# Kernel optimization log

Hardware: AMD Instinct MI355X
Metric: run time of the kernel (lower is better)

Reference implementation:

```python
import jax, jax.numpy as jnp
import numpy as np

TREE_DEPTH = 10
TOTAL = 2 ** (TREE_DEPTH + 1) - 1  # 2047 nodes per tree
G = 64                              # graphs per batch
N = G * TOTAL                       # 131008 nodes
E = 2 * N                           # 262016 directed edges
H = 256                             # h_dim
HALF = H // 2
L = 4                               # num_layers
LABELS = 32
OUT = 32
BN_EPS = 1e-5
LN_EPS = 1e-5


def setup_inputs() -> dict:
    key = jax.random.key(0)
    ks = jax.random.split(key, 16)
    x = jnp.stack([jax.random.randint(ks[0], (N,), 0, TOTAL),
                   jax.random.randint(ks[1], (N,), 0, LABELS)], axis=1)
    edge_src = jax.random.randint(ks[2], (E,), 0, N)
    edge_dst = jax.random.randint(ks[3], (E,), 0, N)
    edge_weight = jax.random.uniform(ks[4], (E,), dtype=jnp.float32)
    batch = jnp.arange(N, dtype=jnp.int64) // TOTAL          # node -> graph id
    root_index = jnp.arange(G, dtype=jnp.int64) * TOTAL      # one root per graph
    s = 0.02
    emb_node = jax.random.normal(ks[5], (TOTAL, HALF), dtype=jnp.float32) * s
    emb_label = jax.random.normal(ks[6], (LABELS, HALF), dtype=jnp.float32) * s
    w = 1.0 / np.sqrt(H)
    W1 = jax.random.normal(ks[7], (L, H, H), dtype=jnp.float32) * w
    b1 = jnp.zeros((L, H), dtype=jnp.float32)
    g1 = jnp.ones((L, H), dtype=jnp.float32)
    be1 = jnp.zeros((L, H), dtype=jnp.float32)
    W2 = jax.random.normal(ks[8], (L, H, H), dtype=jnp.float32) * w
    b2 = jnp.zeros((L, H), dtype=jnp.float32)
    g2 = jnp.ones((L, H), dtype=jnp.float32)
    be2 = jnp.zeros((L, H), dtype=jnp.float32)
    ln_g = jnp.ones((L, H), dtype=jnp.float32)
    ln_b = jnp.zeros((L, H), dtype=jnp.float32)
    Wout = jax.random.normal(ks[9], (OUT, H), dtype=jnp.float32) * w
    return {"x": x, "edge_src": edge_src, "edge_dst": edge_dst,
            "edge_weight": edge_weight, "batch": batch, "root_index": root_index,
            "emb_node": emb_node, "emb_label": emb_label,
            "W1": W1, "b1": b1, "g1": g1, "be1": be1,
            "W2": W2, "b2": b2, "g2": g2, "be2": be2,
            "ln_g": ln_g, "ln_b": ln_b, "Wout": Wout}


def _batchnorm(h, g, b):
    # BatchNorm1d, training-mode batch statistics over the node dim
    m = h.mean(axis=0)
    v = h.var(axis=0)
    return g * (h - m) * jax.lax.rsqrt(v + BN_EPS) + b


def _layernorm(h, g, b):
    m = h.mean(axis=-1, keepdims=True)
    v = h.var(axis=-1, keepdims=True)
    return g * (h - m) * jax.lax.rsqrt(v + LN_EPS) + b


def reference(x, edge_src, edge_dst, edge_weight, batch, root_index,
              emb_node, emb_label, W1, b1, g1, be1, W2, b2, g2, be2,
              ln_g, ln_b, Wout):
    # BiEmbedding_cat: concat of two h/2 embeddings
    h = jnp.concatenate([emb_node[x[:, 0]], emb_label[x[:, 1]]], axis=-1)  # [N,H]
    target_roots = root_index[batch]  # all-nodes->root targets for last layer
    for i in range(L):
        if i == L - 1:  # last_layer_fully_adjacent: every node sends to its root
            agg = jnp.zeros_like(h).at[target_roots].add(h)
        else:
            agg = jnp.zeros_like(h).at[edge_dst].add(h[edge_src] * edge_weight[:, None])
        m = h + agg  # GIN with eps=0: (1+eps)*x + sum_j w_ij x_j
        m = jax.nn.relu(_batchnorm(m @ W1[i].T + b1[i], g1[i], be1[i]))
        m = jax.nn.relu(_batchnorm(m @ W2[i].T + b2[i], g2[i], be2[i]))
        # use_activation: relu (idempotent after the MLP's trailing relu)
        h = h + m  # use_residual
        h = _layernorm(h, ln_g[i], ln_b[i])
    roots_x = h[root_index]  # [G,H] root readout
    return roots_x @ Wout.T  # [G,OUT], bias-free out layer
```

## Files before the change

kernel.cpp:

```cpp
#include <hip/hip_runtime.h>
#include <stdint.h>

#define NN 131008
#define NPAD 131072
#define EE 262016
#define HD 256
#define GG 64
#define TT 2047

typedef __attribute__((ext_vector_type(8))) short bfrag;
typedef __attribute__((ext_vector_type(4))) float f32x4;

__device__ __forceinline__ float bflo(unsigned u){ union{unsigned i; float f;} v; v.i = u<<16; return v.f; }
__device__ __forceinline__ float bfhi(unsigned u){ union{unsigned i; float f;} v; v.i = u & 0xffff0000u; return v.f; }
__device__ __forceinline__ unsigned short f2bf(float f){
  union{unsigned i; float fl;} v; v.fl = f; unsigned i = v.i;
  return (unsigned short)((i + 0x7fffu + ((i>>16)&1u)) >> 16);
}
__device__ __forceinline__ unsigned pack2(float a, float b){
  return (unsigned)f2bf(a) | ((unsigned)f2bf(b)<<16);
}
__device__ __forceinline__ void gload16(const void* g, void* s){
  __builtin_amdgcn_global_load_lds((__attribute__((address_space(1))) void*)g,
                                   (__attribute__((address_space(3))) void*)s, 16, 0, 0);
}

__device__ __forceinline__ short bnrelu1(short t, float a, float c){
  union{unsigned i; float f;} v; v.i = ((unsigned)(unsigned short)t) << 16;
  return (short)f2bf(fmaxf(a*v.f + c, 0.f));
}
__device__ __forceinline__ bfrag bn8(bfrag t, float4 a0, float4 a1, float4 c0, float4 c1){
  bfrag r;
  r[0]=bnrelu1(t[0],a0.x,c0.x); r[1]=bnrelu1(t[1],a0.y,c0.y);
  r[2]=bnrelu1(t[2],a0.z,c0.z); r[3]=bnrelu1(t[3],a0.w,c0.w);
  r[4]=bnrelu1(t[4],a1.x,c1.x); r[5]=bnrelu1(t[5],a1.y,c1.y);
  r[6]=bnrelu1(t[6],a1.z,c1.z); r[7]=bnrelu1(t[7],a1.w,c1.w);
  return r;
}

__device__ __forceinline__ void atomic_add_bf16x2(unsigned short* p, float a, float b){
#if __has_builtin(__builtin_amdgcn_global_atomic_fadd_v2bf16)
  typedef __attribute__((ext_vector_type(2))) short s16x2;
  s16x2 v; v.x = (short)f2bf(a); v.y = (short)f2bf(b);
  __builtin_amdgcn_global_atomic_fadd_v2bf16((__attribute__((address_space(1))) s16x2*)p, v);
#else
  unsigned* up = (unsigned*)p;
  unsigned old = *up, assumed;
  do {
    assumed = old;
    unsigned nv = pack2(bflo(assumed) + a, bfhi(assumed) + b);
    old = atomicCAS(up, assumed, nv);
  } while (old != assumed);
#endif
}

__global__ void k_convw(const float* __restrict__ W1, const float* __restrict__ W2,
                        unsigned short* __restrict__ wbf){
  int idx = blockIdx.x*256 + threadIdx.x;
  float v = (idx < 262144) ? W1[idx] : W2[idx - 262144];
  wbf[idx] = f2bf(v);
}

__global__ void k_embed(const int* __restrict__ x, const float* __restrict__ en,
                        const float* __restrict__ el,
                        unsigned short* __restrict__ hbf){
  size_t i8 = ((size_t)blockIdx.x*256 + threadIdx.x) << 3;
  int row = (int)(i8 >> 8); int k = (int)(i8 & 255);
  uint4 o;
  if (row < NN){
    const float* src = (k < 128) ? en + (size_t)x[2*row]*128 + k
                                 : el + (size_t)x[2*row+1]*128 + (k-128);
    float4 v0 = *(const float4*)src;
    float4 v1 = *(const float4*)(src + 4);
    o.x = pack2(v0.x, v0.y); o.y = pack2(v0.z, v0.w);
    o.z = pack2(v1.x, v1.y); o.w = pack2(v1.z, v1.w);
  } else { o.x = o.y = o.z = o.w = 0u; }
  *(uint4*)(hbf + i8) = o;
}

__global__ void k_hist(const int* __restrict__ ed, int* __restrict__ deg){
  int e = blockIdx.x*256 + threadIdx.x;
  if (e < EE) atomicAdd(&deg[ed[e]], 1);
}
__global__ void k_scan_block(const int* __restrict__ deg, int* __restrict__ start,
                             int* __restrict__ bsum){
  __shared__ int sh[256];
  int t = threadIdx.x;
  int i = blockIdx.x*256 + t;
  int v = deg[i];
  int val = v; sh[t] = val; __syncthreads();
  for (int off = 1; off < 256; off <<= 1){
    int add = (t >= off) ? sh[t-off] : 0;
    __syncthreads();
    val += add; sh[t] = val;
    __syncthreads();
  }
  start[i] = val - v;
  if (t == 255) bsum[blockIdx.x] = val;
}
__global__ void k_scan_top(int* __restrict__ bsum){
  __shared__ int sh[512];
  int t = threadIdx.x;
  int v = bsum[t];
  int val = v; sh[t] = val; __syncthreads();
  for (int off = 1; off < 512; off <<= 1){
    int add = (t >= off) ? sh[t-off] : 0;
    __syncthreads();
    val += add; sh[t] = val;
    __syncthreads();
  }
  bsum[t] = val - v;
}
__global__ void k_initcur(int* __restrict__ start, const int* __restrict__ bsum,
                          int* __restrict__ cursor){
  int i = blockIdx.x*256 + threadIdx.x;
  int v = start[i] + bsum[i >> 8];
  start[i] = v; cursor[i] = v;
}
__global__ void k_fill(const int* __restrict__ es, const int* __restrict__ ed,
                       const float* __restrict__ ew,
                       int* __restrict__ cursor, uint2* __restrict__ pairs){
  int e = blockIdx.x*256 + threadIdx.x;
  if (e < EE){
    int d = ed[e];
    int pos = atomicAdd(&cursor[d], 1);
    uint2 p; p.x = (unsigned)es[e];
    union{float f; unsigned u;} w; w.f = ew[e];
    p.y = w.u;
    pairs[pos] = p;
  }
}

__global__ void k_gather(const int* __restrict__ deg, const int* __restrict__ start,
                         const uint2* __restrict__ pairs,
                         const unsigned short* __restrict__ hbf,
                         unsigned short* __restrict__ mbf){
  int half = threadIdx.x >> 5, lane32 = threadIdx.x & 31;
  int row = blockIdx.x*8 + half;
  size_t base = (size_t)row*HD + (lane32 << 3);
  uint4 o;
  if (row < NN){
    uint4 hv = *(const uint4*)(hbf + base);
    float a0 = bflo(hv.x), a1 = bfhi(hv.x), a2 = bflo(hv.y), a3 = bfhi(hv.y);
    float a4 = bflo(hv.z), a5 = bfhi(hv.z), a6 = bflo(hv.w), a7 = bfhi(hv.w);
    int d = deg[row], s = start[row];
    for (int j = 0; j < d; ++j){
      uint2 pr = pairs[s + j];
      union{unsigned u; float f;} wg; wg.u = pr.y;
      uint4 sv = *(const uint4*)(hbf + (size_t)pr.x*HD + (lane32 << 3));
      a0 += bflo(sv.x)*wg.f; a1 += bfhi(sv.x)*wg.f;
      a2 += bflo(sv.y)*wg.f; a3 += bfhi(sv.y)*wg.f;
      a4 += bflo(sv.z)*wg.f; a5 += bfhi(sv.z)*wg.f;
      a6 += bflo(sv.w)*wg.f; a7 += bfhi(sv.w)*wg.f;
    }
    o.x = pack2(a0, a1); o.y = pack2(a2, a3);
    o.z = pack2(a4, a5); o.w = pack2(a6, a7);
  } else { o.x = o.y = o.z = o.w = 0u; }
  *(uint4*)(mbf + base) = o;
}

__global__ void k_rootsum(const unsigned short* __restrict__ hbf, unsigned short* __restrict__ m){
  int g = blockIdx.x >> 4, ch = blockIdx.x & 15;
  int col = threadIdx.x * 2;
  int nr = (ch == 15) ? 127 : 128;
  const unsigned short* p = hbf + ((size_t)g*TT + ch*128)*HD + col;
  float a = 0.f, b = 0.f;
  for (int r = 0; r < nr; ++r){
    unsigned u = *(const unsigned*)(p + (size_t)r*HD);
    a += bflo(u); b += bfhi(u);
  }
  atomic_add_bf16x2(m + (size_t)g*TT*HD + col, a, b);
}

__global__ __launch_bounds__(512) void k_gemm(const unsigned short* __restrict__ A,
                                              const unsigned short* __restrict__ B,
                                              unsigned short* __restrict__ C,
                                              float* __restrict__ gsum, float* __restrict__ gsq){
  __shared__ unsigned short As[128*64];
  __shared__ unsigned short Bs[256*64];
  __shared__ float rs[256];
  __shared__ float rq[256];
  const int tid = threadIdx.x, lane = tid & 63, w = tid >> 6;
  const int wr = w >> 2, wc = w & 3;
  const int mb = blockIdx.x;
  if (tid < 256){ rs[tid] = 0.f; rq[tid] = 0.f; }
  f32x4 acc[4][4];
  f32x4 zz = {0.f, 0.f, 0.f, 0.f};
#pragma unroll
  for (int a = 0; a < 4; ++a)
#pragma unroll
    for (int b = 0; b < 4; ++b) acc[a][b] = zz;

  for (int kt = 0; kt < 4; ++kt){
    __syncthreads();
#pragma unroll
    for (int it = 0; it < 2; ++it){
      int ci = it*512 + tid;
      int row = ci >> 3, cp = ci & 7;
      int cl = cp ^ (row & 7);
      gload16(A + ((size_t)mb*128 + row)*HD + kt*64 + cl*8, &As[ci*8]);
    }
#pragma unroll
    for (int it = 0; it < 4; ++it){
      int ci = it*512 + tid;
      int row = ci >> 3, cp = ci & 7;
      int cl = cp ^ (row & 7);
      gload16(B + (size_t)row*HD + kt*64 + cl*8, &Bs[ci*8]);
    }
    __syncthreads();
    bfrag af[4][2], bfv[4][2];
    {
      const int q = lane >> 4, r15 = lane & 15, r7 = lane & 7;
#pragma unroll
      for (int rt = 0; rt < 4; ++rt){
        int ra = wr*64 + rt*16 + r15;
        int rb = wc*64 + rt*16 + r15;
#pragma unroll
        for (int hf = 0; hf < 2; ++hf){
          af[rt][hf]  = *(const bfrag*)&As[ra*64 + (((q + 4*hf) ^ r7) << 3)];
          bfv[rt][hf] = *(const bfrag*)&Bs[rb*64 + (((q + 4*hf) ^ r7) << 3)];
        }
      }
    }
#pragma unroll
    for (int hf = 0; hf < 2; ++hf)
#pragma unroll
      for (int rt = 0; rt < 4; ++rt)
#pragma unroll
        for (int ct = 0; ct < 4; ++ct)
          acc[rt][ct] = __builtin_amdgcn_mfma_f32_16x16x32_bf16(af[rt][hf], bfv[ct][hf], acc[rt][ct], 0, 0, 0);
  }

  const int lr0 = wr*64 + (lane >> 4)*4;
  const int lc0 = wc*64 + (lane & 15);
  float cs[4] = {0.f,0.f,0.f,0.f}, cq[4] = {0.f,0.f,0.f,0.f};
#pragma unroll
  for (int rt = 0; rt < 4; ++rt){
#pragma unroll
    for (int ct = 0; ct < 4; ++ct){
#pragma unroll
      for (int i = 0; i < 4; ++i){
        size_t grow = (size_t)mb*128 + lr0 + rt*16 + i;
        float v = acc[rt][ct][i];
        C[grow*HD + lc0 + ct*16] = f2bf(v);
        if (grow < NN){ cs[ct] += v; cq[ct] += v*v; }
      }
    }
  }
#pragma unroll
  for (int ct = 0; ct < 4; ++ct){
    float s = cs[ct], q = cq[ct];
    s += __shfl_xor(s, 16); s += __shfl_xor(s, 32);
    q += __shfl_xor(q, 16); q += __shfl_xor(q, 32);
    if ((lane >> 4) == 0){
      atomicAdd(&rs[lc0 + ct*16], s);
      atomicAdd(&rq[lc0 + ct*16], q);
    }
  }
  __syncthreads();
  if (tid < 256){
    atomicAdd(&gsum[tid], rs[tid]);
    atomicAdd(&gsq[tid], rq[tid]);
  }
}

__global__ __launch_bounds__(512) void k_gemm2(const unsigned short* __restrict__ T,
                                               const float* __restrict__ sum1,
                                               const float* __restrict__ sq1,
                                               const float* __restrict__ g1v,
                                               const float* __restrict__ be1v,
                                               const unsigned short* __restrict__ B,
                                               unsigned short* __restrict__ C,
                                               float* __restrict__ gsum, float* __restrict__ gsq){
  __shared__ unsigned short As[128*64];
  __shared__ unsigned short Bs[256*64];
  __shared__ float rs[256];
  __shared__ float rq[256];
  __shared__ float acf[256];
  __shared__ float ccf[256];
  const int tid = threadIdx.x, lane = tid & 63, w = tid >> 6;
  const int wr = w >> 2, wc = w & 3;
  const int mb = blockIdx.x;
  if (tid < 256){
    rs[tid] = 0.f; rq[tid] = 0.f;
    const float inv_n = 1.f/(float)NN;
    float mean = sum1[tid] * inv_n;
    float var  = fmaxf(sq1[tid] * inv_n - mean*mean, 0.f);
    float aj   = g1v[tid] * rsqrtf(var + 1e-5f);
    acf[tid] = aj;
    ccf[tid] = be1v[tid] - aj*mean;
  }
  f32x4 acc[4][4];
  f32x4 zz = {0.f, 0.f, 0.f, 0.f};
#pragma unroll
  for (int a = 0; a < 4; ++a)
#pragma unroll
    for (int b = 0; b < 4; ++b) acc[a][b] = zz;

  for (int kt = 0; kt < 4; ++kt){
    __syncthreads();
#pragma unroll
    for (int it = 0; it < 2; ++it){
      int ci = it*512 + tid;
      int row = ci >> 3, cp = ci & 7;
      int cl = cp ^ (row & 7);
      gload16(T + ((size_t)mb*128 + row)*HD + kt*64 + cl*8, &As[ci*8]);
    }
#pragma unroll
    for (int it = 0; it < 4; ++it){
      int ci = it*512 + tid;
      int row = ci >> 3, cp = ci & 7;
      int cl = cp ^ (row & 7);
      gload16(B + (size_t)row*HD + kt*64 + cl*8, &Bs[ci*8]);
    }
    __syncthreads();
#pragma unroll
    for (int it = 0; it < 2; ++it){
      int ci = it*512 + tid;
      int row = ci >> 3, cp = ci & 7;
      int kb = (cp ^ (row & 7)) << 3;
      bfrag v = *(const bfrag*)&As[ci*8];
      float4 a0 = *(const float4*)&acf[kt*64 + kb];
      float4 a1 = *(const float4*)&acf[kt*64 + kb + 4];
      float4 c0 = *(const float4*)&ccf[kt*64 + kb];
      float4 c1 = *(const float4*)&ccf[kt*64 + kb + 4];
      *(bfrag*)&As[ci*8] = bn8(v, a0, a1, c0, c1);
    }
    __syncthreads();
    bfrag af[4][2], bfv[4][2];
    {
      const int q = lane >> 4, r15 = lane & 15, r7 = lane & 7;
#pragma unroll
      for (int rt = 0; rt < 4; ++rt){
        int ra = wr*64 + rt*16 + r15;
        int rb = wc*64 + rt*16 + r15;
#pragma unroll
        for (int hf = 0; hf < 2; ++hf){
          af[rt][hf]  = *(const bfrag*)&As[ra*64 + (((q + 4*hf) ^ r7) << 3)];
          bfv[rt][hf] = *(const bfrag*)&Bs[rb*64 + (((q + 4*hf) ^ r7) << 3)];
        }
      }
    }
#pragma unroll
    for (int hf = 0; hf < 2; ++hf)
#pragma unroll
      for (int rt = 0; rt < 4; ++rt)
#pragma unroll
        for (int ct = 0; ct < 4; ++ct)
          acc[rt][ct] = __builtin_amdgcn_mfma_f32_16x16x32_bf16(af[rt][hf], bfv[ct][hf], acc[rt][ct], 0, 0, 0);
  }

  const int lr0 = wr*64 + (lane >> 4)*4;
  const int lc0 = wc*64 + (lane & 15);
  float cs[4] = {0.f,0.f,0.f,0.f}, cq[4] = {0.f,0.f,0.f,0.f};
#pragma unroll
  for (int rt = 0; rt < 4; ++rt){
#pragma unroll
    for (int ct = 0; ct < 4; ++ct){
#pragma unroll
      for (int i = 0; i < 4; ++i){
        size_t grow = (size_t)mb*128 + lr0 + rt*16 + i;
        float v = acc[rt][ct][i];
        C[grow*HD + lc0 + ct*16] = f2bf(v);
        if (grow < NN){ cs[ct] += v; cq[ct] += v*v; }
      }
    }
  }
#pragma unroll
  for (int ct = 0; ct < 4; ++ct){
    float s = cs[ct], q = cq[ct];
    s += __shfl_xor(s, 16); s += __shfl_xor(s, 32);
    q += __shfl_xor(q, 16); q += __shfl_xor(q, 32);
    if ((lane >> 4) == 0){
      atomicAdd(&rs[lc0 + ct*16], s);
      atomicAdd(&rq[lc0 + ct*16], q);
    }
  }
  __syncthreads();
  if (tid < 256){
    atomicAdd(&gsum[tid], rs[tid]);
    atomicAdd(&gsq[tid], rq[tid]);
  }
}

__device__ __forceinline__ void coef4(float4 s4, float4 q4, float4 g4, float4 b4,
                                      float4& a, float4& c){
  const float inv_n = 1.f/(float)NN;
  float m0 = s4.x*inv_n, m1 = s4.y*inv_n, m2 = s4.z*inv_n, m3 = s4.w*inv_n;
  float i0 = rsqrtf(fmaxf(q4.x*inv_n - m0*m0, 0.f) + 1e-5f);
  float i1 = rsqrtf(fmaxf(q4.y*inv_n - m1*m1, 0.f) + 1e-5f);
  float i2 = rsqrtf(fmaxf(q4.z*inv_n - m2*m2, 0.f) + 1e-5f);
  float i3 = rsqrtf(fmaxf(q4.w*inv_n - m3*m3, 0.f) + 1e-5f);
  a.x = g4.x*i0; a.y = g4.y*i1; a.z = g4.z*i2; a.w = g4.w*i3;
  c.x = b4.x - a.x*m0; c.y = b4.y - a.y*m1; c.z = b4.z - a.z*m2; c.w = b4.w - a.w*m3;
}

__global__ void k_fuse(const unsigned short* t2,
                       const float* __restrict__ sum, const float* __restrict__ sq,
                       const float* __restrict__ g, const float* __restrict__ be,
                       const float* __restrict__ lg, const float* __restrict__ lb,
                       unsigned short* __restrict__ hbf, unsigned short* mbf,
                       int writem){
  int half = threadIdx.x >> 5, lane32 = threadIdx.x & 31;
  size_t row = (size_t)blockIdx.x*8 + half;
  int col = lane32 << 3;
  size_t base = row*HD + col;
  uint4 o;
  if (row < NN){
    float4 av0, cv0, av1, cv1;
    coef4(*(const float4*)(sum + col),     *(const float4*)(sq + col),
          *(const float4*)(g + col),       *(const float4*)(be + col),     av0, cv0);
    coef4(*(const float4*)(sum + col + 4), *(const float4*)(sq + col + 4),
          *(const float4*)(g + col + 4),   *(const float4*)(be + col + 4), av1, cv1);
    uint4 tv = *(const uint4*)(t2 + base);
    uint4 hv = *(const uint4*)(hbf + base);
    float r0 = bflo(hv.x) + fmaxf(av0.x*bflo(tv.x) + cv0.x, 0.f);
    float r1 = bfhi(hv.x) + fmaxf(av0.y*bfhi(tv.x) + cv0.y, 0.f);
    float r2 = bflo(hv.y) + fmaxf(av0.z*bflo(tv.y) + cv0.z, 0.f);
    float r3 = bfhi(hv.y) + fmaxf(av0.w*bfhi(tv.y) + cv0.w, 0.f);
    float r4 = bflo(hv.z) + fmaxf(av1.x*bflo(tv.z) + cv1.x, 0.f);
    float r5 = bfhi(hv.z) + fmaxf(av1.y*bfhi(tv.z) + cv1.y, 0.f);
    float r6 = bflo(hv.w) + fmaxf(av1.z*bflo(tv.w) + cv1.z, 0.f);
    float r7 = bfhi(hv.w) + fmaxf(av1.w*bfhi(tv.w) + cv1.w, 0.f);
    float s  = r0+r1+r2+r3+r4+r5+r6+r7;
    float qq = r0*r0+r1*r1+r2*r2+r3*r3+r4*r4+r5*r5+r6*r6+r7*r7;
#pragma unroll
    for (int d = 1; d < 32; d <<= 1){ s += __shfl_xor(s, d); qq += __shfl_xor(qq, d); }
    float mean = s * (1.f/256.f);
    float var  = fmaxf(qq * (1.f/256.f) - mean*mean, 0.f);
    float inv  = rsqrtf(var + 1e-5f);
    float4 gv0 = *(const float4*)(lg + col), gv1 = *(const float4*)(lg + col + 4);
    float4 bv0 = *(const float4*)(lb + col), bv1 = *(const float4*)(lb + col + 4);
    o.x = pack2(gv0.x*(r0 - mean)*inv + bv0.x, gv0.y*(r1 - mean)*inv + bv0.y);
    o.y = pack2(gv0.z*(r2 - mean)*inv + bv0.z, gv0.w*(r3 - mean)*inv + bv0.w);
    o.z = pack2(gv1.x*(r4 - mean)*inv + bv1.x, gv1.y*(r5 - mean)*inv + bv1.y);
    o.w = pack2(gv1.z*(r6 - mean)*inv + bv1.z, gv1.w*(r7 - mean)*inv + bv1.w);
  } else {
    o.x = o.y = o.z = o.w = 0u;
  }
  *(uint4*)(hbf + base) = o;
  if (writem) *(uint4*)(mbf + base) = o;
}

__global__ void k_readout(const unsigned short* __restrict__ hbf, const float* __restrict__ Wo,
                          float* __restrict__ out){
  int g = blockIdx.x;
  int w = threadIdx.x >> 6, lane = threadIdx.x & 63;
  uint2 hv = *(const uint2*)(hbf + (size_t)g*TT*HD + (lane<<2));
  float h0 = bflo(hv.x), h1 = bfhi(hv.x), h2 = bflo(hv.y), h3 = bfhi(hv.y);
#pragma unroll
  for (int oo = 0; oo < 8; ++oo){
    int o = w*8 + oo;
    float4 wv = *(const float4*)(Wo + (size_t)o*HD + (lane<<2));
    float p = h0*wv.x + h1*wv.y + h2*wv.z + h3*wv.w;
#pragma unroll
    for (int d = 1; d < 64; d <<= 1) p += __shfl_xor(p, d);
    if (lane == 0) out[g*32 + o] = p;
  }
}

extern "C" void kernel_launch(void* const* d_in, const int* in_sizes, int n_in,
                              void* d_out, int out_size, void* d_ws, size_t ws_size,
                              hipStream_t stream){
  const int*   x   = (const int*)d_in[0];
  const int*   es  = (const int*)d_in[1];
  const int*   ed  = (const int*)d_in[2];
  const float* ew  = (const float*)d_in[3];
  const float* en  = (const float*)d_in[6];
  const float* el  = (const float*)d_in[7];
  const float* W1  = (const float*)d_in[8];
  const float* g1  = (const float*)d_in[10];
  const float* be1 = (const float*)d_in[11];
  const float* W2  = (const float*)d_in[12];
  const float* g2  = (const float*)d_in[14];
  const float* be2 = (const float*)d_in[15];
  const float* lg  = (const float*)d_in[16];
  const float* lb  = (const float*)d_in[17];
  const float* Wo  = (const float*)d_in[18];

  char* ws = (char*)d_ws;
  unsigned short* hbf = (unsigned short*)ws;
  unsigned short* mbf = (unsigned short*)(ws + 67108864);
  unsigned short* t   = (unsigned short*)(ws + 134217728);
  unsigned short* wbf = (unsigned short*)(ws + 201326592);
  float* stats  = (float*)(ws + 202375168);
  int*   deg    = (int*)  (ws + 202391552);
  int*   start  = (int*)  (ws + 202915840);
  int*   cursor = (int*)  (ws + 203440128);
  int*   bsum   = (int*)  (ws + 203964416);
  uint2* pairs  = (uint2*)(ws + 203968512);

  hipMemsetAsync(stats, 0, 16384 + 524288, stream);
  k_convw<<<2048,  256, 0, stream>>>(W1, W2, wbf);
  k_embed<<<16384, 256, 0, stream>>>(x, en, el, hbf);

  k_hist      <<<1024, 256, 0, stream>>>(ed, deg);
  k_scan_block<<<512,  256, 0, stream>>>(deg, start, bsum);
  k_scan_top  <<<1,    512, 0, stream>>>(bsum);
  k_initcur   <<<512,  256, 0, stream>>>(start, bsum, cursor);
  k_fill      <<<1024, 256, 0, stream>>>(es, ed, ew, cursor, pairs);

  for (int i = 0; i < 4; ++i){
    if (i < 3) k_gather <<<16384, 256, 0, stream>>>(deg, start, pairs, hbf, mbf);
    else       k_rootsum<<<1024,  128, 0, stream>>>(hbf, mbf);

    float* s1 = stats + (2*i)*512;
    float* s2 = stats + (2*i+1)*512;
    k_gemm <<<1024, 512, 0, stream>>>(mbf, wbf + i*65536, t, s1, s1 + 256);
    k_gemm2<<<1024, 512, 0, stream>>>(t, s1, s1 + 256, g1 + i*256, be1 + i*256,
                                      wbf + 262144 + i*65536, mbf, s2, s2 + 256);
    k_fuse <<<16384, 256, 0, stream>>>(mbf, s2, s2 + 256, g2 + i*256, be2 + i*256,
                                       lg + i*256, lb + i*256, hbf, mbf, (i == 2) ? 1 : 0);
  }

  k_readout<<<64, 256, 0, stream>>>(hbf, Wo, (float*)d_out);
  (void)in_sizes; (void)n_in; (void)out_size; (void)ws_size;
}
```

Baseline: 886.0 us.

## Prefetch next A tile into registers during MFMA in both GEMM kernels

Restructures the k-loop of the two GEMM kernels so the next K-slice of A is loaded into registers while the current slice's MFMAs run. After compute it is written to LDS (with the batchnorm transform applied in gemm2), and the B slice is issued via LDS-direct loads. This hides global load latency and drops a barrier per iteration. It costs extra registers, and the B gload into LDS is issued just before the next barrier, so its latency is still only partly overlapped.

```diff
diff --git a/kernel.cpp b/kernel.cpp
--- a/kernel.cpp
+++ b/kernel.cpp
@@ -191,23 +191,27 @@
 #pragma unroll
     for (int b = 0; b < 4; ++b) acc[a][b] = zz;
 
+#pragma unroll
+  for (int it = 0; it < 2; ++it){
+    int ci = it*512 + tid, row = ci >> 3, cl = (ci & 7) ^ (row & 7);
+    gload16(A + ((size_t)mb*128 + row)*HD + cl*8, &As[ci*8]);
+  }
+#pragma unroll
+  for (int it = 0; it < 4; ++it){
+    int ci = it*512 + tid, row = ci >> 3, cl = (ci & 7) ^ (row & 7);
+    gload16(B + (size_t)row*HD + cl*8, &Bs[ci*8]);
+  }
+
+  uint4 pa[2];
   for (int kt = 0; kt < 4; ++kt){
     __syncthreads();
-#pragma unroll
-    for (int it = 0; it < 2; ++it){
-      int ci = it*512 + tid;
-      int row = ci >> 3, cp = ci & 7;
-      int cl = cp ^ (row & 7);
-      gload16(A + ((size_t)mb*128 + row)*HD + kt*64 + cl*8, &As[ci*8]);
-    }
-#pragma unroll
-    for (int it = 0; it < 4; ++it){
-      int ci = it*512 + tid;
-      int row = ci >> 3, cp = ci & 7;
-      int cl = cp ^ (row & 7);
-      gload16(B + (size_t)row*HD + kt*64 + cl*8, &Bs[ci*8]);
-    }
-    __syncthreads();
+    if (kt < 3){
+#pragma unroll
+      for (int it = 0; it < 2; ++it){
+        int ci = it*512 + tid, row = ci >> 3, cl = (ci & 7) ^ (row & 7);
+        pa[it] = *(const uint4*)(A + ((size_t)mb*128 + row)*HD + (kt+1)*64 + cl*8);
+      }
+    }
     bfrag af[4][2], bfv[4][2];
     {
       const int q = lane >> 4, r15 = lane & 15, r7 = lane & 7;
@@ -229,6 +233,19 @@
 #pragma unroll
         for (int ct = 0; ct < 4; ++ct)
           acc[rt][ct] = __builtin_amdgcn_mfma_f32_16x16x32_bf16(af[rt][hf], bfv[ct][hf], acc[rt][ct], 0, 0, 0);
+    __syncthreads();
+    if (kt < 3){
+#pragma unroll
+      for (int it = 0; it < 2; ++it){
+        int ci = it*512 + tid;
+        *(uint4*)&As[ci*8] = pa[it];
+      }
+#pragma unroll
+      for (int it = 0; it < 4; ++it){
+        int ci = it*512 + tid, row = ci >> 3, cl = (ci & 7) ^ (row & 7);
+        gload16(B + (size_t)row*HD + (kt+1)*64 + cl*8, &Bs[ci*8]);
+      }
+    }
   }
 
   const int lr0 = wr*64 + (lane >> 4)*4;
@@ -281,6 +298,13 @@
   const int tid = threadIdx.x, lane = tid & 63, w = tid >> 6;
   const int wr = w >> 2, wc = w & 3;
   const int mb = blockIdx.x;
+
+  uint4 pa[2];
+#pragma unroll
+  for (int it = 0; it < 2; ++it){
+    int ci = it*512 + tid, row = ci >> 3, cl = (ci & 7) ^ (row & 7);
+    pa[it] = *(const uint4*)(T + ((size_t)mb*128 + row)*HD + cl*8);
+  }
   if (tid < 256){
     rs[tid] = 0.f; rq[tid] = 0.f;
     const float inv_n = 1.f/(float)NN;
@@ -290,6 +314,22 @@
     acf[tid] = aj;
     ccf[tid] = be1v[tid] - aj*mean;
   }
+  __syncthreads();
+#pragma unroll
+  for (int it = 0; it < 2; ++it){
+    int ci = it*512 + tid, row = ci >> 3, cl = (ci & 7) ^ (row & 7);
+    int kb = cl*8;
+    bfrag v = *(bfrag*)&pa[it];
+    float4 a0 = *(const float4*)&acf[kb], a1 = *(const float4*)&acf[kb + 4];
+    float4 c0 = *(const float4*)&ccf[kb], c1 = *(const float4*)&ccf[kb + 4];
+    *(bfrag*)&As[ci*8] = bn8(v, a0, a1, c0, c1);
+  }
+#pragma unroll
+  for (int it = 0; it < 4; ++it){
+    int ci = it*512 + tid, row = ci >> 3, cl = (ci & 7) ^ (row & 7);
+    gload16(B + (size_t)row*HD + cl*8, &Bs[ci*8]);
+  }
+
   f32x4 acc[4][4];
   f32x4 zz = {0.f, 0.f, 0.f, 0.f};
 #pragma unroll
@@ -299,34 +339,13 @@
 
   for (int kt = 0; kt < 4; ++kt){
     __syncthreads();
-#pragma unroll
-    for (int it = 0; it < 2; ++it){
-      int ci = it*512 + tid;
-      int row = ci >> 3, cp = ci & 7;
-      int cl = cp ^ (row & 7);
-      gload16(T + ((size_t)mb*128 + row)*HD + kt*64 + cl*8, &As[ci*8]);
-    }
-#pragma unroll
-    for (int it = 0; it < 4; ++it){
-      int ci = it*512 + tid;
-      int row = ci >> 3, cp = ci & 7;
-      int cl = cp ^ (row & 7);
-      gload16(B + (size_t)row*HD + kt*64 + cl*8, &Bs[ci*8]);
-    }
-    __syncthreads();
-#pragma unroll
-    for (int it = 0; it < 2; ++it){
-      int ci = it*512 + tid;
-      int row = ci >> 3, cp = ci & 7;
-      int kb = (cp ^ (row & 7)) << 3;
-      bfrag v = *(const bfrag*)&As[ci*8];
-      float4 a0 = *(const float4*)&acf[kt*64 + kb];
-      float4 a1 = *(const float4*)&acf[kt*64 + kb + 4];
-      float4 c0 = *(const float4*)&ccf[kt*64 + kb];
-      float4 c1 = *(const float4*)&ccf[kt*64 + kb + 4];
-      *(bfrag*)&As[ci*8] = bn8(v, a0, a1, c0, c1);
-    }
-    __syncthreads();
+    if (kt < 3){
+#pragma unroll
+      for (int it = 0; it < 2; ++it){
+        int ci = it*512 + tid, row = ci >> 3, cl = (ci & 7) ^ (row & 7);
+        pa[it] = *(const uint4*)(T + ((size_t)mb*128 + row)*HD + (kt+1)*64 + cl*8);
+      }
+    }
     bfrag af[4][2], bfv[4][2];
     {
       const int q = lane >> 4, r15 = lane & 15, r7 = lane & 7;
@@ -348,6 +367,23 @@
 #pragma unroll
         for (int ct = 0; ct < 4; ++ct)
           acc[rt][ct] = __builtin_amdgcn_mfma_f32_16x16x32_bf16(af[rt][hf], bfv[ct][hf], acc[rt][ct], 0, 0, 0);
+    __syncthreads();
+    if (kt < 3){
+#pragma unroll
+      for (int it = 0; it < 2; ++it){
+        int ci = it*512 + tid, row = ci >> 3, cl = (ci & 7) ^ (row & 7);
+        int kb = (kt+1)*64 + cl*8;
+        bfrag v = *(bfrag*)&pa[it];
+        float4 a0 = *(const float4*)&acf[kb], a1 = *(const float4*)&acf[kb + 4];
+        float4 c0 = *(const float4*)&ccf[kb], c1 = *(const float4*)&ccf[kb + 4];
+        *(bfrag*)&As[ci*8] = bn8(v, a0, a1, c0, c1);
+      }
+#pragma unroll
+      for (int it = 0; it < 4; ++it){
+        int ci = it*512 + tid, row = ci >> 3, cl = (ci & 7) ^ (row & 7);
+        gload16(B + (size_t)row*HD + (kt+1)*64 + cl*8, &Bs[ci*8]);
+      }
+    }
   }
 
   const int lr0 = wr*64 + (lane >> 4)*4;
```

Result: no change. 900.5 us (+1.6%).

## Fuse neighbor gather aggregation into first GEMM's A-tile load

Applied to the files above, without the earlier changes.

Removes the standalone gather kernel for layers 0-2. The first MLP GEMM now builds its A tile in shared memory by summing each node's own row with its weighted neighbor rows, one 64-column k-slice at a time. This avoids writing the aggregated matrix to global memory and reading it back. In exchange, the irregular gather latency now sits inside the GEMM's k-loop, which can stall the MFMA work and reduce overlap. The per-row degree and start indices are loaded once per block.

```diff
diff --git a/kernel.cpp b/kernel.cpp
--- a/kernel.cpp
+++ b/kernel.cpp
@@ -131,34 +131,6 @@
   }
 }
 
-__global__ void k_gather(const int* __restrict__ deg, const int* __restrict__ start,
-                         const uint2* __restrict__ pairs,
-                         const unsigned short* __restrict__ hbf,
-                         unsigned short* __restrict__ mbf){
-  int half = threadIdx.x >> 5, lane32 = threadIdx.x & 31;
-  int row = blockIdx.x*8 + half;
-  size_t base = (size_t)row*HD + (lane32 << 3);
-  uint4 o;
-  if (row < NN){
-    uint4 hv = *(const uint4*)(hbf + base);
-    float a0 = bflo(hv.x), a1 = bfhi(hv.x), a2 = bflo(hv.y), a3 = bfhi(hv.y);
-    float a4 = bflo(hv.z), a5 = bfhi(hv.z), a6 = bflo(hv.w), a7 = bfhi(hv.w);
-    int d = deg[row], s = start[row];
-    for (int j = 0; j < d; ++j){
-      uint2 pr = pairs[s + j];
-      union{unsigned u; float f;} wg; wg.u = pr.y;
-      uint4 sv = *(const uint4*)(hbf + (size_t)pr.x*HD + (lane32 << 3));
-      a0 += bflo(sv.x)*wg.f; a1 += bfhi(sv.x)*wg.f;
-      a2 += bflo(sv.y)*wg.f; a3 += bfhi(sv.y)*wg.f;
-      a4 += bflo(sv.z)*wg.f; a5 += bfhi(sv.z)*wg.f;
-      a6 += bflo(sv.w)*wg.f; a7 += bfhi(sv.w)*wg.f;
-    }
-    o.x = pack2(a0, a1); o.y = pack2(a2, a3);
-    o.z = pack2(a4, a5); o.w = pack2(a6, a7);
-  } else { o.x = o.y = o.z = o.w = 0u; }
-  *(uint4*)(mbf + base) = o;
-}
-
 __global__ void k_rootsum(const unsigned short* __restrict__ hbf, unsigned short* __restrict__ m){
   int g = blockIdx.x >> 4, ch = blockIdx.x & 15;
   int col = threadIdx.x * 2;
@@ -206,6 +178,129 @@
       int row = ci >> 3, cp = ci & 7;
       int cl = cp ^ (row & 7);
       gload16(B + (size_t)row*HD + kt*64 + cl*8, &Bs[ci*8]);
+    }
+    __syncthreads();
+    bfrag af[4][2], bfv[4][2];
+    {
+      const int q = lane >> 4, r15 = lane & 15, r7 = lane & 7;
+#pragma unroll
+      for (int rt = 0; rt < 4; ++rt){
+        int ra = wr*64 + rt*16 + r15;
+        int rb = wc*64 + rt*16 + r15;
+#pragma unroll
+        for (int hf = 0; hf < 2; ++hf){
+          af[rt][hf]  = *(const bfrag*)&As[ra*64 + (((q + 4*hf) ^ r7) << 3)];
+          bfv[rt][hf] = *(const bfrag*)&Bs[rb*64 + (((q + 4*hf) ^ r7) << 3)];
+        }
+      }
+    }
+#pragma unroll
+    for (int hf = 0; hf < 2; ++hf)
+#pragma unroll
+      for (int rt = 0; rt < 4; ++rt)
+#pragma unroll
+        for (int ct = 0; ct < 4; ++ct)
+          acc[rt][ct] = __builtin_amdgcn_mfma_f32_16x16x32_bf16(af[rt][hf], bfv[ct][hf], acc[rt][ct], 0, 0, 0);
+  }
+
+  const int lr0 = wr*64 + (lane >> 4)*4;
+  const int lc0 = wc*64 + (lane & 15);
+  float cs[4] = {0.f,0.f,0.f,0.f}, cq[4] = {0.f,0.f,0.f,0.f};
+#pragma unroll
+  for (int rt = 0; rt < 4; ++rt){
+#pragma unroll
+    for (int ct = 0; ct < 4; ++ct){
+#pragma unroll
+      for (int i = 0; i < 4; ++i){
+        size_t grow = (size_t)mb*128 + lr0 + rt*16 + i;
+        float v = acc[rt][ct][i];
+        C[grow*HD + lc0 + ct*16] = f2bf(v);
+        if (grow < NN){ cs[ct] += v; cq[ct] += v*v; }
+      }
+    }
+  }
+#pragma unroll
+  for (int ct = 0; ct < 4; ++ct){
+    float s = cs[ct], q = cq[ct];
+    s += __shfl_xor(s, 16); s += __shfl_xor(s, 32);
+    q += __shfl_xor(q, 16); q += __shfl_xor(q, 32);
+    if ((lane >> 4) == 0){
+      atomicAdd(&rs[lc0 + ct*16], s);
+      atomicAdd(&rq[lc0 + ct*16], q);
+    }
+  }
+  __syncthreads();
+  if (tid < 256){
+    atomicAdd(&gsum[tid], rs[tid]);
+    atomicAdd(&gsq[tid], rq[tid]);
+  }
+}
+
+__global__ __launch_bounds__(512) void k_gemm1g(const int* __restrict__ deg,
+                                                const int* __restrict__ start,
+                                                const uint2* __restrict__ pairs,
+                                                const unsigned short* __restrict__ hbf,
+                                                const unsigned short* __restrict__ B,
+                                                unsigned short* __restrict__ C,
+                                                float* __restrict__ gsum, float* __restrict__ gsq){
+  __shared__ unsigned short As[128*64];
+  __shared__ unsigned short Bs[256*64];
+  __shared__ float rs[256];
+  __shared__ float rq[256];
+  const int tid = threadIdx.x, lane = tid & 63, w = tid >> 6;
+  const int wr = w >> 2, wc = w & 3;
+  const int mb = blockIdx.x;
+  if (tid < 256){ rs[tid] = 0.f; rq[tid] = 0.f; }
+
+  const int row0 = tid >> 3,         cl0 = (tid & 7) ^ (row0 & 7);
+  const int row1 = (512+tid) >> 3,   cl1 = ((512+tid) & 7) ^ (row1 & 7);
+  const int g0 = mb*128 + row0, g1 = mb*128 + row1;
+  int d0 = 0, s0 = 0, d1 = 0, s1 = 0;
+  if (g0 < NN){ d0 = deg[g0]; s0 = start[g0]; }
+  if (g1 < NN){ d1 = deg[g1]; s1 = start[g1]; }
+
+  f32x4 acc[4][4];
+  f32x4 zz = {0.f, 0.f, 0.f, 0.f};
+#pragma unroll
+  for (int a = 0; a < 4; ++a)
+#pragma unroll
+    for (int b = 0; b < 4; ++b) acc[a][b] = zz;
+
+  for (int kt = 0; kt < 4; ++kt){
+    __syncthreads();
+#pragma unroll
+    for (int it = 0; it < 4; ++it){
+      int ci = it*512 + tid;
+      int row = ci >> 3, cp = ci & 7;
+      int cl = cp ^ (row & 7);
+      gload16(B + (size_t)row*HD + kt*64 + cl*8, &Bs[ci*8]);
+    }
+#pragma unroll
+    for (int c = 0; c < 2; ++c){
+      int ci   = c ? (512+tid) : tid;
+      int grow = c ? g1 : g0;
+      int cl   = c ? cl1 : cl0;
+      int d    = c ? d1 : d0;
+      int s    = c ? s1 : s0;
+      uint4 o;
+      if (grow < NN){
+        size_t coff = (size_t)kt*64 + cl*8;
+        uint4 hv = *(const uint4*)(hbf + (size_t)grow*HD + coff);
+        float a0 = bflo(hv.x), a1 = bfhi(hv.x), a2 = bflo(hv.y), a3 = bfhi(hv.y);
+        float a4 = bflo(hv.z), a5 = bfhi(hv.z), a6 = bflo(hv.w), a7 = bfhi(hv.w);
+        for (int j = 0; j < d; ++j){
+          uint2 pr = pairs[s + j];
+          union{unsigned u; float f;} wg; wg.u = pr.y;
+          uint4 sv = *(const uint4*)(hbf + (size_t)pr.x*HD + coff);
+          a0 += bflo(sv.x)*wg.f; a1 += bfhi(sv.x)*wg.f;
+          a2 += bflo(sv.y)*wg.f; a3 += bfhi(sv.y)*wg.f;
+          a4 += bflo(sv.z)*wg.f; a5 += bfhi(sv.z)*wg.f;
+          a6 += bflo(sv.w)*wg.f; a7 += bfhi(sv.w)*wg.f;
+        }
+        o.x = pack2(a0, a1); o.y = pack2(a2, a3);
+        o.z = pack2(a4, a5); o.w = pack2(a6, a7);
+      } else { o.x = o.y = o.z = o.w = 0u; }
+      *(uint4*)&As[ci*8] = o;
     }
     __syncthreads();
     bfrag af[4][2], bfv[4][2];
@@ -501,12 +596,15 @@
   k_fill      <<<1024, 256, 0, stream>>>(es, ed, ew, cursor, pairs);
 
   for (int i = 0; i < 4; ++i){
-    if (i < 3) k_gather <<<16384, 256, 0, stream>>>(deg, start, pairs, hbf, mbf);
-    else       k_rootsum<<<1024,  128, 0, stream>>>(hbf, mbf);
-
     float* s1 = stats + (2*i)*512;
     float* s2 = stats + (2*i+1)*512;
-    k_gemm <<<1024, 512, 0, stream>>>(mbf, wbf + i*65536, t, s1, s1 + 256);
+    if (i < 3){
+      k_gemm1g<<<1024, 512, 0, stream>>>(deg, start, pairs, hbf,
+                                         wbf + i*65536, t, s1, s1 + 256);
+    } else {
+      k_rootsum<<<1024, 128, 0, stream>>>(hbf, mbf);
+      k_gemm   <<<1024, 512, 0, stream>>>(mbf, wbf + i*65536, t, s1, s1 + 256);
+    }
     k_gemm2<<<1024, 512, 0, stream>>>(t, s1, s1 + 256, g1 + i*256, be1 + i*256,
                                       wbf + 262144 + i*65536, mbf, s2, s2 + 256);
     k_fuse <<<16384, 256, 0, stream>>>(mbf, s2, s2 + 256, g2 + i*256, be2 + i*256,
```

New measurement: 1.058 ms. +19.4%, slower.
